# Optimization experiments

Hardware: AMD Instinct MI355X
Metric: run time of the kernel (lower is better)

Reference implementation:

```python
import jax, jax.numpy as jnp
import numpy as np

NT, NC, D = 20000, 80000, 256
SLOPE = 0.01  # torch F.leaky_relu default negative_slope


def _lrelu(x):
    return jnp.where(x >= 0, x, SLOPE * x)


def setup_inputs() -> dict:
    key = jax.random.key(0)
    ks = jax.random.split(key, 20)
    sc = 1.0 / np.sqrt(D)

    def W(k):
        return jax.random.normal(k, (D, D), jnp.float32) * sc

    return {
        "feat_table": jax.random.normal(ks[0], (NT, D), jnp.float32),
        "feat_column": jax.random.normal(ks[1], (NC, D), jnp.float32),
        "W_t2c": W(ks[2]), "b_t2c": jnp.zeros((D,), jnp.float32),
        "W_c2t": W(ks[3]), "b_c2t": jnp.zeros((D,), jnp.float32),
        "W_c2c": W(ks[4]), "b_c2c": jnp.zeros((D,), jnp.float32),
        "W_t2t": W(ks[5]), "b_t2t": jnp.zeros((D,), jnp.float32),
        "W_h": W(ks[6]), "b_h": jnp.zeros((D,), jnp.float32),
        "src_t2c": jax.random.randint(ks[7], (320000,), 0, NT, jnp.int32),
        "dst_t2c": jax.random.randint(ks[8], (320000,), 0, NC, jnp.int32),
        "src_c2t": jax.random.randint(ks[9], (320000,), 0, NC, jnp.int32),
        "dst_c2t": jax.random.randint(ks[10], (320000,), 0, NT, jnp.int32),
        "src_c2c": jax.random.randint(ks[11], (640000,), 0, NC, jnp.int32),
        "dst_c2c": jax.random.randint(ks[12], (640000,), 0, NC, jnp.int32),
        "src_t2t": jax.random.randint(ks[13], (160000,), 0, NT, jnp.int32),
        "dst_t2t": jax.random.randint(ks[14], (160000,), 0, NT, jnp.int32),
    }


def _mean_agg(Wh, src, dst, n_dst):
    # copy_u + mean: gather src messages, segment-mean into dst nodes
    s = jax.ops.segment_sum(Wh[src], dst, num_segments=n_dst)  # [n_dst, D]
    c = jax.ops.segment_sum(jnp.ones(src.shape, Wh.dtype), dst, num_segments=n_dst)
    return s / jnp.maximum(c, 1.0)[:, None]


def reference(feat_table, feat_column,
              W_t2c, b_t2c, W_c2t, b_c2t, W_c2c, b_c2c, W_t2t, b_t2t,
              W_h, b_h,
              src_t2c, dst_t2c, src_c2t, dst_c2t,
              src_c2c, dst_c2c, src_t2t, dst_t2t):
    # per-etype Linear + leaky_relu on source-node features
    Wh_t2c = _lrelu(feat_table @ W_t2c.T + b_t2c)
    Wh_c2t = _lrelu(feat_column @ W_c2t.T + b_c2t)
    Wh_c2c = _lrelu(feat_column @ W_c2c.T + b_c2c)
    Wh_t2t = _lrelu(feat_table @ W_t2t.T + b_t2t)

    # per-etype mean aggregation, then cross-etype 'mean' (2 etypes per ntype)
    h_table = 0.5 * (_mean_agg(Wh_c2t, src_c2t, dst_c2t, NT)
                     + _mean_agg(Wh_t2t, src_t2t, dst_t2t, NT))
    h_column = 0.5 * (_mean_agg(Wh_t2c, src_t2c, dst_t2c, NC)
                      + _mean_agg(Wh_c2c, src_c2c, dst_c2c, NC))

    out_table = _lrelu(h_table @ W_h.T + b_h) + feat_table
    out_column = _lrelu(h_column @ W_h.T + b_h) + feat_column
    return out_table, out_column
```

## Files before the change

### kernel.cpp

```cpp
#include <hip/hip_runtime.h>

#define D 256
#define SLOPE 0.01f

#define BSH 9
#define BSZ 512
#define NBMAX 160
#define EPB 8192

typedef __attribute__((ext_vector_type(8))) short bf16x8;
typedef __attribute__((ext_vector_type(4))) float f32x4;

__device__ __forceinline__ float bfbits2f(unsigned int hi) {
  return __builtin_bit_cast(float, hi);
}
__device__ __forceinline__ unsigned short f2bf(float f) {
  unsigned u = __builtin_bit_cast(unsigned, f);
  u += 0x7fffu + ((u >> 16) & 1u);
  return (unsigned short)(u >> 16);
}
__device__ __forceinline__ float lrelu(float x) {
  return (x >= 0.f) ? x : SLOPE * x;
}

__device__ __forceinline__ void gld_lds16(const void* g, void* l) {
  __builtin_amdgcn_global_load_lds(
      (const __attribute__((address_space(1))) unsigned int*)g,
      (__attribute__((address_space(3))) unsigned int*)l, 16, 0, 0);
}

__global__ void cast2_kernel(const float* __restrict__ i0,
                             unsigned short* __restrict__ o0, int n40,
                             const float* __restrict__ i1,
                             unsigned short* __restrict__ o1, int n41) {
  int a = blockIdx.y;
  const float* in = a ? i1 : i0;
  unsigned short* out = a ? o1 : o0;
  int n4 = a ? n41 : n40;
  int i = blockIdx.x * blockDim.x + threadIdx.x;
  if (i >= n4) return;
  float4 v = ((const float4*)in)[i];
  ushort4 o;
  o.x = f2bf(v.x); o.y = f2bf(v.y); o.z = f2bf(v.z); o.w = f2bf(v.w);
  ((ushort4*)out)[i] = o;
}

__global__ void cast5_kernel(const float* w0, const float* w1, const float* w2,
                             const float* w3, const float* w4,
                             unsigned short* o0, unsigned short* o1,
                             unsigned short* o2, unsigned short* o3,
                             unsigned short* o4) {
  int a = blockIdx.y;
  const float* in = a == 0 ? w0 : a == 1 ? w1 : a == 2 ? w2 : a == 3 ? w3 : w4;
  unsigned short* out = a == 0 ? o0 : a == 1 ? o1 : a == 2 ? o2 : a == 3 ? o3 : o4;
  int i = blockIdx.x * blockDim.x + threadIdx.x;
  float4 v = ((const float4*)in)[i];
  ushort4 o;
  o.x = f2bf(v.x); o.y = f2bf(v.y); o.z = f2bf(v.z); o.w = f2bf(v.w);
  ((ushort4*)out)[i] = o;
}


__device__ __forceinline__ void stage_A(unsigned short* Xs,
                                        const unsigned short* __restrict__ A,
                                        int M, int mblk) {
  const int t = threadIdx.x;
  const int w = t >> 6, lane = t & 63;
#pragma unroll
  for (int i = 0; i < 8; i++) {
    const int m = (i * 4 + w) * 2 + (lane >> 5);
    int row = mblk + m;
    if (row > M - 1) row = M - 1;
    const int jsrc = (lane & 31) ^ (m & 7);
    gld_lds16(A + (size_t)row * D + jsrc * 8, &Xs[(i * 4 + w) * 512]);
  }
}

template <int MODE, bool SYNC>
__device__ __forceinline__ void gemm_compute(
    const unsigned short* Xs, const unsigned short* __restrict__ B,
    const float* __restrict__ bias, const float* __restrict__ residual,
    unsigned short* __restrict__ outb, float* __restrict__ outf, int M,
    int mblk) {
  const int t = threadIdx.x;
  const int w = t >> 6, lane = t & 63;
  const int fr = lane & 15;
  const int jb = lane >> 4;

  bf16x8 wf[4][8];
  {
    const unsigned short* wp = B + (size_t)(w * 64 + fr) * D + jb * 8;
#pragma unroll
    for (int nt = 0; nt < 4; nt++)
#pragma unroll
      for (int k0 = 0; k0 < 8; k0++)
        wf[nt][k0] = *(const bf16x8*)(wp + nt * 16 * D + k0 * 32);
  }

  if (SYNC) {
    asm volatile("s_waitcnt vmcnt(0)" ::: "memory");
    __syncthreads();
  }

  f32x4 acc[4][4];
#pragma unroll
  for (int i = 0; i < 4; i++)
#pragma unroll
    for (int j = 0; j < 4; j++) acc[i][j] = (f32x4){0.f, 0.f, 0.f, 0.f};

  const int r = fr & 7;
#pragma unroll
  for (int k0 = 0; k0 < 8; k0++) {
    bf16x8 xf[4];
#pragma unroll
    for (int mt = 0; mt < 4; mt++) {
      const int ml = mt * 16 + fr;
      xf[mt] = *(const bf16x8*)&Xs[ml * 256 + (((k0 * 4 + jb) ^ r) * 8)];
    }
#pragma unroll
    for (int mt = 0; mt < 4; mt++)
#pragma unroll
      for (int nt = 0; nt < 4; nt++)
        acc[mt][nt] = __builtin_amdgcn_mfma_f32_16x16x32_bf16(
            wf[nt][k0], xf[mt], acc[mt][nt], 0, 0, 0);
  }

  const int n0 = w * 64 + jb * 4;
  float4 bv[4];
#pragma unroll
  for (int nt = 0; nt < 4; nt++) bv[nt] = *(const float4*)&bias[n0 + nt * 16];

#pragma unroll
  for (int mt = 0; mt < 4; mt++) {
    const int m = mblk + mt * 16 + fr;
    if (m < M) {
      if (MODE == 1) {
        float4 rv[4];
#pragma unroll
        for (int nt = 0; nt < 4; nt++)
          rv[nt] = *(const float4*)&residual[(size_t)m * D + n0 + nt * 16];
#pragma unroll
        for (int nt = 0; nt < 4; nt++) {
          float4 o;
          o.x = lrelu(acc[mt][nt][0] + bv[nt].x) + rv[nt].x;
          o.y = lrelu(acc[mt][nt][1] + bv[nt].y) + rv[nt].y;
          o.z = lrelu(acc[mt][nt][2] + bv[nt].z) + rv[nt].z;
          o.w = lrelu(acc[mt][nt][3] + bv[nt].w) + rv[nt].w;
          *(float4*)&outf[(size_t)m * D + n0 + nt * 16] = o;
        }
      } else {
#pragma unroll
        for (int nt = 0; nt < 4; nt++) {
          ushort4 o;
          o.x = f2bf(lrelu(acc[mt][nt][0] + bv[nt].x));
          o.y = f2bf(lrelu(acc[mt][nt][1] + bv[nt].y));
          o.z = f2bf(lrelu(acc[mt][nt][2] + bv[nt].z));
          o.w = f2bf(lrelu(acc[mt][nt][3] + bv[nt].w));
          *(ushort4*)&outb[(size_t)m * D + n0 + nt * 16] = o;
        }
      }
    }
  }
}

__global__ __launch_bounds__(256, 2) void gemm0_pair(
    const unsigned short* __restrict__ A0, const unsigned short* __restrict__ A1,
    const unsigned short* __restrict__ B00, const unsigned short* __restrict__ B01,
    const unsigned short* __restrict__ B10, const unsigned short* __restrict__ B11,
    const float* b00, const float* b01, const float* b10, const float* b11,
    unsigned short* o00, unsigned short* o01, unsigned short* o10,
    unsigned short* o11, int M0, int M1) {
  __shared__ __attribute__((aligned(16))) unsigned short Xs[64 * 256];
  int a = blockIdx.y;
  const unsigned short* A = a ? A1 : A0;
  int M = a ? M1 : M0;
  int mblk = blockIdx.x * 64;
  if (mblk >= M) return;
  stage_A(Xs, A, M, mblk);
  gemm_compute<0, true>(Xs, a ? B10 : B00, a ? b10 : b00, nullptr,
                        a ? o10 : o00, nullptr, M, mblk);
  gemm_compute<0, false>(Xs, a ? B11 : B01, a ? b11 : b01, nullptr,
                         a ? o11 : o01, nullptr, M, mblk);
}

__global__ __launch_bounds__(256, 2) void gemm1_dual(
    const unsigned short* __restrict__ A0, const unsigned short* __restrict__ A1,
    const unsigned short* __restrict__ Bw, const float* bh,
    const float* __restrict__ r0, const float* __restrict__ r1,
    float* __restrict__ o0, float* __restrict__ o1, int M0, int M1) {
  __shared__ __attribute__((aligned(16))) unsigned short Xs[64 * 256];
  int a = blockIdx.y;
  const unsigned short* A = a ? A1 : A0;
  int M = a ? M1 : M0;
  int mblk = blockIdx.x * 64;
  if (mblk >= M) return;
  stage_A(Xs, A, M, mblk);
  gemm_compute<1, true>(Xs, Bw, bh, a ? r1 : r0, nullptr, a ? o1 : o0, M, mblk);
}

__global__ __launch_bounds__(256) void bucketCount_kernel(
    const int* d0, int n0, const int* d1, int n1, const int* d2, int n2,
    const int* d3, int n3, int* __restrict__ bcnt) {
  int a = blockIdx.y;
  const int* dst = a == 0 ? d0 : a == 1 ? d1 : a == 2 ? d2 : d3;
  int n = a == 0 ? n0 : a == 1 ? n1 : a == 2 ? n2 : n3;
  int blk = blockIdx.x;
  if (blk * EPB >= n) return;
  int t = threadIdx.x;
  __shared__ int cnt[NBMAX];
  if (t < NBMAX) cnt[t] = 0;
  __syncthreads();
  int i0 = blk * EPB + t;
#pragma unroll 4
  for (int it = 0; it < EPB / 256; it++) {
    int i = i0 + it * 256;
    if (i < n) atomicAdd(&cnt[dst[i] >> BSH], 1);
  }
  __syncthreads();
  if (t < NBMAX && cnt[t]) atomicAdd(&bcnt[a * NBMAX + t], cnt[t]);
}

__global__ __launch_bounds__(256) void bucketScan_kernel(
    const int* __restrict__ bcnt, int* __restrict__ bbase,
    int* o0, int n0, int e0, int* o1, int n1, int e1,
    int* o2, int n2, int e2, int* o3, int n3, int e3) {
  __shared__ int s[256];
  int t = threadIdx.x;
  for (int a = 0; a < 4; a++) {
    int v = (t < NBMAX) ? bcnt[a * NBMAX + t] : 0;
    s[t] = v;
    __syncthreads();
    for (int off = 1; off < 256; off <<= 1) {
      int u = (t >= off) ? s[t - off] : 0;
      __syncthreads();
      s[t] += u;
      __syncthreads();
    }
    if (t < NBMAX)
      bbase[a * (NBMAX + 1) + t] = s[t] - v;
    else if (t == NBMAX)
      bbase[a * (NBMAX + 1) + NBMAX] = s[NBMAX - 1];
    __syncthreads();
  }
  if (t == 0) { o0[n0] = e0; o1[n1] = e1; o2[n2] = e2; o3[n3] = e3; }
}

__global__ __launch_bounds__(256) void bucketA_kernel(
    const int* s0, const int* d0, int n0, unsigned* t0,
    const int* s1, const int* d1, int n1, unsigned* t1,
    const int* s2, const int* d2, int n2, unsigned* t2,
    const int* s3, const int* d3, int n3, unsigned* t3,
    const int* __restrict__ bbase, int* __restrict__ bcur) {
  int a = blockIdx.y;
  const int* src = a == 0 ? s0 : a == 1 ? s1 : a == 2 ? s2 : s3;
  const int* dst = a == 0 ? d0 : a == 1 ? d1 : a == 2 ? d2 : d3;
  int n = a == 0 ? n0 : a == 1 ? n1 : a == 2 ? n2 : n3;
  unsigned* temp = a == 0 ? t0 : a == 1 ? t1 : a == 2 ? t2 : t3;

  int blk = blockIdx.x;
  if (blk * EPB >= n) return;
  int t = threadIdx.x;
  __shared__ int cnt[NBMAX];
  __shared__ int lbase[NBMAX];
  if (t < NBMAX) cnt[t] = 0;
  __syncthreads();

  int i0 = blk * EPB + t;
#pragma unroll 4
  for (int it = 0; it < EPB / 256; it++) {
    int i = i0 + it * 256;
    if (i < n) atomicAdd(&cnt[dst[i] >> BSH], 1);
  }
  __syncthreads();
  if (t < NBMAX) {
    int c = cnt[t];
    int g = c ? atomicAdd(&bcur[a * NBMAX + t], c) : 0;
    lbase[t] = g + bbase[a * (NBMAX + 1) + t];
    cnt[t] = 0;
  }
  __syncthreads();
#pragma unroll 4
  for (int it = 0; it < EPB / 256; it++) {
    int i = i0 + it * 256;
    if (i < n) {
      int d = dst[i];
      int b = d >> BSH;
      int rk = atomicAdd(&cnt[b], 1);
      temp[lbase[b] + rk] = ((unsigned)src[i] << BSH) | (unsigned)(d & (BSZ - 1));
    }
  }
}

__global__ __launch_bounds__(256) void bucketFinal_kernel(
    const unsigned* t0, int* o0, int* e0, int m0,
    const unsigned* t1, int* o1, int* e1, int m1,
    const unsigned* t2, int* o2, int* e2, int m2,
    const unsigned* t3, int* o3, int* e3, int m3,
    const int* __restrict__ bbase) {
  int a = blockIdx.y;
  const unsigned* temp = a == 0 ? t0 : a == 1 ? t1 : a == 2 ? t2 : t3;
  int* offs = a == 0 ? o0 : a == 1 ? o1 : a == 2 ? o2 : o3;
  int* elist = a == 0 ? e0 : a == 1 ? e1 : a == 2 ? e2 : e3;
  int nn = a == 0 ? m0 : a == 1 ? m1 : a == 2 ? m2 : m3;

  int nb = (nn + BSZ - 1) >> BSH;
  int b = blockIdx.x;
  if (b >= nb) return;
  int lo = bbase[a * (NBMAX + 1) + b];
  int hi = bbase[a * (NBMAX + 1) + b + 1];
  int t = threadIdx.x;

  __shared__ int cnt[BSZ];
  __shared__ int psum[BSZ];
  __shared__ int sm[256];
  cnt[t] = 0; cnt[t + 256] = 0;
  __syncthreads();
  for (int i = lo + t; i < hi; i += 256)
    atomicAdd(&cnt[temp[i] & (BSZ - 1)], 1);
  __syncthreads();
  int c0 = cnt[2 * t], c1 = cnt[2 * t + 1];
  int s = c0 + c1;
  sm[t] = s;
  __syncthreads();
  for (int off = 1; off < 256; off <<= 1) {
    int u = (t >= off) ? sm[t - off] : 0;
    __syncthreads();
    sm[t] += u;
    __syncthreads();
  }
  int ex = sm[t] - s;
  psum[2 * t] = ex;
  psum[2 * t + 1] = ex + c0;
  cnt[2 * t] = 0; cnt[2 * t + 1] = 0;
  __syncthreads();

  int node0 = b << BSH;
  if (node0 + 2 * t < nn) offs[node0 + 2 * t] = lo + psum[2 * t];
  if (node0 + 2 * t + 1 < nn) offs[node0 + 2 * t + 1] = lo + psum[2 * t + 1];

  for (int i = lo + t; i < hi; i += 256) {
    unsigned v = temp[i];
    int d = v & (BSZ - 1);
    int rk = atomicAdd(&cnt[d], 1);
    elist[lo + psum[d] + rk] = (int)(v >> BSH);
  }
}

__device__ __forceinline__ void add8(float* acc, uint4 p) {
  acc[0] += bfbits2f(p.x << 16);
  acc[1] += bfbits2f(p.x & 0xffff0000u);
  acc[2] += bfbits2f(p.y << 16);
  acc[3] += bfbits2f(p.y & 0xffff0000u);
  acc[4] += bfbits2f(p.z << 16);
  acc[5] += bfbits2f(p.z & 0xffff0000u);
  acc[6] += bfbits2f(p.w << 16);
  acc[7] += bfbits2f(p.w & 0xffff0000u);
}

__global__ __launch_bounds__(256) void aggregate_kernel(
    const unsigned short* __restrict__ WhA, const int* __restrict__ offsA,
    const int* __restrict__ elistA, const unsigned short* __restrict__ WhB,
    const int* __restrict__ offsB, const int* __restrict__ elistB,
    unsigned short* __restrict__ hout, int n) {
  int wave = (blockIdx.x * 256 + threadIdx.x) >> 6;
  int lane = threadIdx.x & 63;
  if (wave >= n) return;
  int half = lane >> 5;
  int l32 = lane & 31;
  size_t coff = (size_t)l32 * 8;

  float accA[8] = {0, 0, 0, 0, 0, 0, 0, 0};
  float accB[8] = {0, 0, 0, 0, 0, 0, 0, 0};
  float scA, scB;

  {
    int e0 = offsA[wave], e1 = offsA[wave + 1];
    scA = 0.5f / fmaxf((float)(e1 - e0), 1.0f);
    int e = e0;
    for (; e + 8 <= e1; e += 8) {
      int s0 = elistA[e + half];
      int s1 = elistA[e + 2 + half];
      int s2 = elistA[e + 4 + half];
      int s3 = elistA[e + 6 + half];
      uint4 p0 = *(const uint4*)(WhA + (size_t)s0 * D + coff);
      uint4 p1 = *(const uint4*)(WhA + (size_t)s1 * D + coff);
      uint4 p2 = *(const uint4*)(WhA + (size_t)s2 * D + coff);
      uint4 p3 = *(const uint4*)(WhA + (size_t)s3 * D + coff);
      add8(accA, p0); add8(accA, p1); add8(accA, p2); add8(accA, p3);
    }
    for (; e + 2 <= e1; e += 2) {
      int s0 = elistA[e + half];
      uint4 p0 = *(const uint4*)(WhA + (size_t)s0 * D + coff);
      add8(accA, p0);
    }
    if (e < e1 && half == 0) {
      int s0 = elistA[e];
      uint4 p0 = *(const uint4*)(WhA + (size_t)s0 * D + coff);
      add8(accA, p0);
    }
  }
  {
    int e0 = offsB[wave], e1 = offsB[wave + 1];
    scB = 0.5f / fmaxf((float)(e1 - e0), 1.0f);
    int e = e0;
    for (; e + 8 <= e1; e += 8) {
      int s0 = elistB[e + half];
      int s1 = elistB[e + 2 + half];
      int s2 = elistB[e + 4 + half];
      int s3 = elistB[e + 6 + half];
      uint4 p0 = *(const uint4*)(WhB + (size_t)s0 * D + coff);
      uint4 p1 = *(const uint4*)(WhB + (size_t)s1 * D + coff);
      uint4 p2 = *(const uint4*)(WhB + (size_t)s2 * D + coff);
      uint4 p3 = *(const uint4*)(WhB + (size_t)s3 * D + coff);
      add8(accB, p0); add8(accB, p1); add8(accB, p2); add8(accB, p3);
    }
    for (; e + 2 <= e1; e += 2) {
      int s0 = elistB[e + half];
      uint4 p0 = *(const uint4*)(WhB + (size_t)s0 * D + coff);
      add8(accB, p0);
    }
    if (e < e1 && half == 0) {
      int s0 = elistB[e];
      uint4 p0 = *(const uint4*)(WhB + (size_t)s0 * D + coff);
      add8(accB, p0);
    }
  }

  float h[8];
#pragma unroll
  for (int j = 0; j < 8; j++) {
    h[j] = accA[j] * scA + accB[j] * scB;
    h[j] += __shfl_down(h[j], 32);
  }
  if (half == 0) {
    uint4 o;
    o.x = (unsigned)f2bf(h[0]) | ((unsigned)f2bf(h[1]) << 16);
    o.y = (unsigned)f2bf(h[2]) | ((unsigned)f2bf(h[3]) << 16);
    o.z = (unsigned)f2bf(h[4]) | ((unsigned)f2bf(h[5]) << 16);
    o.w = (unsigned)f2bf(h[6]) | ((unsigned)f2bf(h[7]) << 16);
    *(uint4*)(hout + (size_t)wave * D + coff) = o;
  }
}

extern "C" void kernel_launch(void* const* d_in, const int* in_sizes, int n_in,
                              void* d_out, int out_size, void* d_ws,
                              size_t ws_size, hipStream_t stream) {
  const float* feat_table = (const float*)d_in[0];
  const float* feat_column = (const float*)d_in[1];
  const float* Wsrc[5] = {(const float*)d_in[2], (const float*)d_in[4],
                          (const float*)d_in[6], (const float*)d_in[8],
                          (const float*)d_in[10]};
  const float* b_t2c = (const float*)d_in[3];
  const float* b_c2t = (const float*)d_in[5];
  const float* b_c2c = (const float*)d_in[7];
  const float* b_t2t = (const float*)d_in[9];
  const float* b_h = (const float*)d_in[11];
  const int* src_t2c = (const int*)d_in[12];
  const int* dst_t2c = (const int*)d_in[13];
  const int* src_c2t = (const int*)d_in[14];
  const int* dst_c2t = (const int*)d_in[15];
  const int* src_c2c = (const int*)d_in[16];
  const int* dst_c2c = (const int*)d_in[17];
  const int* src_t2t = (const int*)d_in[18];
  const int* dst_t2t = (const int*)d_in[19];

  const int NT = in_sizes[0] / D;
  const int NC = in_sizes[1] / D;
  const int E_t2c = in_sizes[12], E_c2t = in_sizes[14];
  const int E_c2c = in_sizes[16], E_t2t = in_sizes[18];

  char* ws = (char*)d_ws;
  size_t cur = 0;
  auto alloc = [&](size_t bytes) -> void* {
    void* p = ws + cur;
    cur += (bytes + 255) & ~(size_t)255;
    return p;
  };
  unsigned short* Wb[5];
  for (int i = 0; i < 5; i++) Wb[i] = (unsigned short*)alloc((size_t)D * D * 2);
  unsigned short* ftb = (unsigned short*)alloc((size_t)NT * D * 2);
  unsigned short* fcb = (unsigned short*)alloc((size_t)NC * D * 2);
  unsigned short* Wh_t2c = (unsigned short*)alloc((size_t)NT * D * 2);
  unsigned short* Wh_c2t = (unsigned short*)alloc((size_t)NC * D * 2);
  unsigned short* Wh_c2c = (unsigned short*)alloc((size_t)NC * D * 2);
  unsigned short* Wh_t2t = (unsigned short*)alloc((size_t)NT * D * 2);
  int* bcnt = (int*)alloc(sizeof(int) * 2 * 4 * NBMAX);
  int* bcur = bcnt + 4 * NBMAX;
  int* bbase = (int*)alloc(sizeof(int) * 4 * (NBMAX + 1));
  int* off_c2t = (int*)alloc(sizeof(int) * (NT + 1));
  int* off_t2t = (int*)alloc(sizeof(int) * (NT + 1));
  int* off_t2c = (int*)alloc(sizeof(int) * (NC + 1));
  int* off_c2c = (int*)alloc(sizeof(int) * (NC + 1));
  int* el_c2t = (int*)alloc(sizeof(int) * E_c2t);
  int* el_t2t = (int*)alloc(sizeof(int) * E_t2t);
  int* el_t2c = (int*)alloc(sizeof(int) * E_t2c);
  int* el_c2c = (int*)alloc(sizeof(int) * E_c2c);

  unsigned* tp_c2t = (unsigned*)ftb;
  unsigned* tp_t2t = tp_c2t + E_c2t;
  unsigned* tp_t2c = tp_t2t + E_t2t;
  unsigned* tp_c2c = tp_t2c + E_t2c;
  unsigned short* h_tab = ftb;
  unsigned short* h_col = fcb;

  hipMemsetAsync(bcnt, 0, sizeof(int) * 2 * 4 * NBMAX, stream);

  {
    dim3 g((D * D / 4 + 255) / 256, 5);
    cast5_kernel<<<g, 256, 0, stream>>>(Wsrc[0], Wsrc[1], Wsrc[2], Wsrc[3],
                                        Wsrc[4], Wb[0], Wb[1], Wb[2], Wb[3],
                                        Wb[4]);
  }
  {
    dim3 g((max(NT, NC) * D / 4 + 255) / 256, 2);
    cast2_kernel<<<g, 256, 0, stream>>>(feat_table, ftb, NT * D / 4,
                                        feat_column, fcb, NC * D / 4);
  }

  {
    dim3 g((max(NT, NC) + 63) / 64, 2);
    gemm0_pair<<<g, 256, 0, stream>>>(
        ftb, fcb, Wb[0], Wb[3], Wb[1], Wb[2], b_t2c, b_t2t, b_c2t, b_c2c,
        Wh_t2c, Wh_t2t, Wh_c2t, Wh_c2c, NT, NC);
  }

  int Emax = max(max(E_c2t, E_t2t), max(E_t2c, E_c2c));
  {
    dim3 g((Emax + EPB - 1) / EPB, 4);
    bucketCount_kernel<<<g, 256, 0, stream>>>(dst_c2t, E_c2t, dst_t2t, E_t2t,
                                              dst_t2c, E_t2c, dst_c2c, E_c2c,
                                              bcnt);
  }
  bucketScan_kernel<<<1, 256, 0, stream>>>(
      bcnt, bbase, off_c2t, NT, E_c2t, off_t2t, NT, E_t2t, off_t2c, NC, E_t2c,
      off_c2c, NC, E_c2c);
  {
    dim3 g((Emax + EPB - 1) / EPB, 4);
    bucketA_kernel<<<g, 256, 0, stream>>>(
        src_c2t, dst_c2t, E_c2t, tp_c2t, src_t2t, dst_t2t, E_t2t, tp_t2t,
        src_t2c, dst_t2c, E_t2c, tp_t2c, src_c2c, dst_c2c, E_c2c, tp_c2c,
        bbase, bcur);
  }
  {
    int nbmax = (max(NT, NC) + BSZ - 1) >> BSH;
    dim3 g(nbmax, 4);
    bucketFinal_kernel<<<g, 256, 0, stream>>>(
        tp_c2t, off_c2t, el_c2t, NT, tp_t2t, off_t2t, el_t2t, NT,
        tp_t2c, off_t2c, el_t2c, NC, tp_c2c, off_c2c, el_c2c, NC, bbase);
  }

  aggregate_kernel<<<(NC + 3) / 4, 256, 0, stream>>>(
      Wh_t2c, off_t2c, el_t2c, Wh_c2c, off_c2c, el_c2c, h_col, NC);
  aggregate_kernel<<<(NT + 3) / 4, 256, 0, stream>>>(
      Wh_c2t, off_c2t, el_c2t, Wh_t2t, off_t2t, el_t2t, h_tab, NT);

  float* out_tab = (float*)d_out;
  float* out_col = out_tab + (size_t)NT * D;
  {
    dim3 g((max(NT, NC) + 63) / 64, 2);
    gemm1_dual<<<g, 256, 0, stream>>>(h_tab, h_col, Wb[4], b_h, feat_table,
                                      feat_column, out_tab, out_col, NT, NC);
  }
}
```

Baseline: 541.6 us.

## Replace paired GEMM0 with persistent double-buffered pipelined kernel

Replaces the two-weights-per-block GEMM0 with a persistent grid of 512 blocks that loop over (weight, row-block) tiles. Each iteration prefetches the next A tile into a second LDS buffer while the current one is computed, overlapping global loads with MFMA work. It also removes the grid padding that left many idle blocks for the smaller table matrix. In exchange, each A tile is loaded twice (once per weight matrix) instead of shared, LDS use doubles per block, and B fragments are reloaded every iteration.

Result: no change. 548.7 us (+1.3%).

```diff
diff --git a/kernel.cpp b/kernel.cpp
--- a/kernel.cpp
+++ b/kernel.cpp
@@ -76,6 +76,112 @@
   }
 }
 
+__global__ __launch_bounds__(256, 2) void gemm0_pipe(
+    const unsigned short* __restrict__ ftb, const unsigned short* __restrict__ fcb,
+    const unsigned short* __restrict__ B0, const unsigned short* __restrict__ B1,
+    const unsigned short* __restrict__ B2, const unsigned short* __restrict__ B3,
+    const float* b0, const float* b1, const float* b2, const float* b3,
+    unsigned short* o0, unsigned short* o1, unsigned short* o2,
+    unsigned short* o3, int M0, int M1, int nbT, int nbC, int G) {
+  __shared__ __attribute__((aligned(16))) unsigned short Xs[2][64 * 256];
+  const int tot = 2 * (nbT + nbC);
+  int tid = blockIdx.x;
+  if (tid >= tot) return;
+
+  const int t = threadIdx.x;
+  const int w = t >> 6, lane = t & 63;
+  const int fr = lane & 15;
+  const int jb = lane >> 4;
+  const int r = fr & 7;
+
+  auto decA = [&](int id) {
+    return (id < 2 * nbT) ? (id / nbT) : (2 + (id - 2 * nbT) / nbC);
+  };
+  auto decM = [&](int id) {
+    return (id < 2 * nbT) ? ((id % nbT) * 64) : (((id - 2 * nbT) % nbC) * 64);
+  };
+
+  {
+    int a = decA(tid);
+    stage_A(Xs[0], (a < 2) ? ftb : fcb, (a < 2) ? M0 : M1, decM(tid));
+  }
+  int cur = 0;
+  for (; tid < tot; tid += G) {
+    const int a = decA(tid);
+    const int mblk = decM(tid);
+    const int M = (a < 2) ? M0 : M1;
+    const unsigned short* B = a == 0 ? B0 : a == 1 ? B1 : a == 2 ? B2 : B3;
+    const float* bias = a == 0 ? b0 : a == 1 ? b1 : a == 2 ? b2 : b3;
+    unsigned short* outb = a == 0 ? o0 : a == 1 ? o1 : a == 2 ? o2 : o3;
+
+    bf16x8 wf[4][8];
+    {
+      const unsigned short* wp = B + (size_t)(w * 64 + fr) * D + jb * 8;
+#pragma unroll
+      for (int nt = 0; nt < 4; nt++)
+#pragma unroll
+        for (int k0 = 0; k0 < 8; k0++)
+          wf[nt][k0] = *(const bf16x8*)(wp + nt * 16 * D + k0 * 32);
+    }
+
+    const int nxt = tid + G;
+    if (nxt < tot) {
+      int a2 = decA(nxt);
+      stage_A(Xs[cur ^ 1], (a2 < 2) ? ftb : fcb, (a2 < 2) ? M0 : M1,
+              decM(nxt));
+      asm volatile("s_waitcnt vmcnt(8)" ::: "memory");
+    } else {
+      asm volatile("s_waitcnt vmcnt(0)" ::: "memory");
+    }
+    __syncthreads();
+
+    const unsigned short* Xc = Xs[cur];
+    f32x4 acc[4][4];
+#pragma unroll
+    for (int i = 0; i < 4; i++)
+#pragma unroll
+      for (int j = 0; j < 4; j++) acc[i][j] = (f32x4){0.f, 0.f, 0.f, 0.f};
+
+#pragma unroll
+    for (int k0 = 0; k0 < 8; k0++) {
+      bf16x8 xf[4];
+#pragma unroll
+      for (int mt = 0; mt < 4; mt++) {
+        const int ml = mt * 16 + fr;
+        xf[mt] = *(const bf16x8*)&Xc[ml * 256 + (((k0 * 4 + jb) ^ r) * 8)];
+      }
+#pragma unroll
+      for (int mt = 0; mt < 4; mt++)
+#pragma unroll
+        for (int nt = 0; nt < 4; nt++)
+          acc[mt][nt] = __builtin_amdgcn_mfma_f32_16x16x32_bf16(
+              wf[nt][k0], xf[mt], acc[mt][nt], 0, 0, 0);
+    }
+
+    const int n0 = w * 64 + jb * 4;
+    float4 bv[4];
+#pragma unroll
+    for (int nt = 0; nt < 4; nt++) bv[nt] = *(const float4*)&bias[n0 + nt * 16];
+#pragma unroll
+    for (int mt = 0; mt < 4; mt++) {
+      const int m = mblk + mt * 16 + fr;
+      if (m < M) {
+#pragma unroll
+        for (int nt = 0; nt < 4; nt++) {
+          ushort4 o;
+          o.x = f2bf(lrelu(acc[mt][nt][0] + bv[nt].x));
+          o.y = f2bf(lrelu(acc[mt][nt][1] + bv[nt].y));
+          o.z = f2bf(lrelu(acc[mt][nt][2] + bv[nt].z));
+          o.w = f2bf(lrelu(acc[mt][nt][3] + bv[nt].w));
+          *(ushort4*)&outb[(size_t)m * D + n0 + nt * 16] = o;
+        }
+      }
+    }
+    __syncthreads();
+    cur ^= 1;
+  }
+}
+
 template <int MODE, bool SYNC>
 __device__ __forceinline__ void gemm_compute(
     const unsigned short* Xs, const unsigned short* __restrict__ B,
@@ -161,26 +267,6 @@
       }
     }
   }
-}
-
-__global__ __launch_bounds__(256, 2) void gemm0_pair(
-    const unsigned short* __restrict__ A0, const unsigned short* __restrict__ A1,
-    const unsigned short* __restrict__ B00, const unsigned short* __restrict__ B01,
-    const unsigned short* __restrict__ B10, const unsigned short* __restrict__ B11,
-    const float* b00, const float* b01, const float* b10, const float* b11,
-    unsigned short* o00, unsigned short* o01, unsigned short* o10,
-    unsigned short* o11, int M0, int M1) {
-  __shared__ __attribute__((aligned(16))) unsigned short Xs[64 * 256];
-  int a = blockIdx.y;
-  const unsigned short* A = a ? A1 : A0;
-  int M = a ? M1 : M0;
-  int mblk = blockIdx.x * 64;
-  if (mblk >= M) return;
-  stage_A(Xs, A, M, mblk);
-  gemm_compute<0, true>(Xs, a ? B10 : B00, a ? b10 : b00, nullptr,
-                        a ? o10 : o00, nullptr, M, mblk);
-  gemm_compute<0, false>(Xs, a ? B11 : B01, a ? b11 : b01, nullptr,
-                         a ? o11 : o01, nullptr, M, mblk);
 }
 
 __global__ __launch_bounds__(256, 2) void gemm1_dual(
@@ -517,11 +603,13 @@
                                         feat_column, fcb, NC * D / 4);
   }
 
-  {
-    dim3 g((max(NT, NC) + 63) / 64, 2);
-    gemm0_pair<<<g, 256, 0, stream>>>(
+  const int nbT = (NT + 63) / 64, nbC = (NC + 63) / 64;
+  {
+    const int G = 512;
+    int tot = 2 * (nbT + nbC);
+    gemm0_pipe<<<min(G, tot), 256, 0, stream>>>(
         ftb, fcb, Wb[0], Wb[3], Wb[1], Wb[2], b_t2c, b_t2t, b_c2t, b_c2c,
-        Wh_t2c, Wh_t2t, Wh_c2t, Wh_c2c, NT, NC);
+        Wh_t2c, Wh_t2t, Wh_c2t, Wh_c2c, NT, NC, nbT, nbC, min(G, tot));
   }
 
   int Emax = max(max(E_c2t, E_t2t), max(E_t2c, E_c2c));
```
